# Kernel tuning notes

Measured on AMD Instinct MI355X. Metric: run time of the kernel, lower is better.

## Reference

```python
import jax, jax.numpy as jnp
import numpy as np
from jax import lax

LN_EPS = 1e-6  # flax LayerNorm default


def _layernorm(x, scale, bias):
    mu = jnp.mean(x, axis=-1, keepdims=True)
    var = jnp.mean(jnp.square(x - mu), axis=-1, keepdims=True)
    return (x - mu) * lax.rsqrt(var + LN_EPS) * scale + bias


def _lstm_layer(c0, h0, Wi, Wh, b, x):
    # x: [B, T, F]; carry c/h: [B, H]; gate order i, f, g, o (flax)
    def step(carry, xt):
        c, h = carry
        z = xt @ Wi + h @ Wh + b  # [B, 4H]
        i, f, g, o = jnp.split(z, 4, axis=-1)
        i = jax.nn.sigmoid(i); f = jax.nn.sigmoid(f)
        g = jnp.tanh(g); o = jax.nn.sigmoid(o)
        c = f * c + i * g
        h = o * jnp.tanh(c)
        return (c, h), h
    (cT, hT), hs = lax.scan(step, (c0, h0), jnp.swapaxes(x, 0, 1))
    return cT, hT, jnp.swapaxes(hs, 0, 1)  # hs: [B, T, H]


def setup_inputs() -> dict:
    key = jax.random.key(0)
    ks = jax.random.split(key, 16)
    B, T, F, H, P, A = 64, 128, 512, 1024, 1024, 32
    s = 0.05
    return {
        "x": jax.random.normal(ks[0], (B, T, F), jnp.float32),
        "c0": jnp.zeros((2, B, H), jnp.float32),
        "h0": jnp.zeros((2, B, H), jnp.float32),
        "W_pre": jax.random.normal(ks[1], (F, P), jnp.float32) * s,
        "b_pre": jnp.zeros((P,), jnp.float32),
        "ln_scale": jnp.ones((P,), jnp.float32),
        "ln_bias": jnp.zeros((P,), jnp.float32),
        "Wi0": jax.random.normal(ks[2], (P, 4 * H), jnp.float32) * s,
        "Wh0": jax.random.normal(ks[3], (H, 4 * H), jnp.float32) * s,
        "b0": jnp.zeros((4 * H,), jnp.float32),
        "Wi1": jax.random.normal(ks[4], (H, 4 * H), jnp.float32) * s,
        "Wh1": jax.random.normal(ks[5], (H, 4 * H), jnp.float32) * s,
        "b1": jnp.zeros((4 * H,), jnp.float32),
        "W_post": jax.random.normal(ks[6], (H, P), jnp.float32) * s,
        "b_post": jnp.zeros((P,), jnp.float32),
        "W_out": jax.random.normal(ks[7], (P, A), jnp.float32) * s,
        "b_out": jnp.zeros((A,), jnp.float32),
        "training": False,
    }


def reference(x, c0, h0, W_pre, b_pre, ln_scale, ln_bias,
              Wi0, Wh0, b0, Wi1, Wh1, b1,
              W_post, b_post, W_out, b_out, training):
    # preprocessing: Dense -> LayerNorm -> relu
    h = jax.nn.relu(_layernorm(x @ W_pre + b_pre, ln_scale, ln_bias))
    # two stacked LSTM layers scanned over time
    c1, h1, h = _lstm_layer(c0[0], h0[0], Wi0, Wh0, b0, h)
    c2, h2, h = _lstm_layer(c0[1], h0[1], Wi1, Wh1, b1, h)
    # postprocessing: Dense -> relu (dropout deterministic => identity)
    h = jax.nn.relu(h @ W_post + b_post)
    logits = h @ W_out + b_out  # [B, T, action_dim]
    new_carry = (jnp.stack([c1, c2]), jnp.stack([h1, h2]))
    return new_carry, logits
```

## Files before the change

kernel.cpp:

```cpp
#include <hip/hip_runtime.h>
#include <hip/hip_bf16.h>
#include <math.h>

typedef __attribute__((ext_vector_type(8))) short short8;
typedef __attribute__((ext_vector_type(4))) float f32x4;
typedef __attribute__((ext_vector_type(4))) unsigned u32x4;
typedef unsigned short u16;
typedef unsigned long long u64;

__device__ __forceinline__ u16 f2bf(float f) {
    union { float f; unsigned u; } v; v.f = f;
    unsigned r = v.u + 0x7fffu + ((v.u >> 16) & 1u);
    return (u16)(r >> 16);
}
__device__ __forceinline__ float bf2f(u16 b) {
    union { unsigned u; float f; } v; v.u = ((unsigned)b) << 16;
    return v.f;
}
__device__ __forceinline__ float fast_sigmoid(float x) {
    return __builtin_amdgcn_rcpf(1.f + __expf(-x));
}
__device__ __forceinline__ float fast_tanh(float x) {
    return 1.f - 2.f * __builtin_amdgcn_rcpf(1.f + __expf(2.f * x));
}
__device__ __forceinline__ u32x4 ldg16(const void* p) {
    u32x4 r;
    asm volatile("global_load_dwordx4 %0, %1, off"
                 : "=v"(r) : "v"(p) : "memory");
    return r;
}


__global__ __launch_bounds__(256) void k_zero(unsigned* p, int n) {
    int i = blockIdx.x * 256 + threadIdx.x;
    if (i < n) p[i] = 0u;
}

__global__ __launch_bounds__(256) void k_cvt(const float* __restrict__ in,
                                             u16* __restrict__ out, int n) {
    int i = blockIdx.x * 256 + threadIdx.x;
    if (i < n) out[i] = f2bf(in[i]);
}

__global__ __launch_bounds__(256) void k_cvt_h(const float* __restrict__ in,
                                               u16* __restrict__ out) {
    int i = blockIdx.x * 256 + threadIdx.x;
    int b = i >> 10, j = i & 1023;
    out[(size_t)(j >> 3) * 512 + b * 8 + (j & 7)] = f2bf(in[i]);
}

__global__ __launch_bounds__(256) void k_transpose(const float* __restrict__ W,
                                                   u16* __restrict__ WT, int K, int N) {
    __shared__ float tile[32][33];
    int n0 = blockIdx.x * 32, k0 = blockIdx.y * 32;
    int tx = threadIdx.x & 31, ty = threadIdx.x >> 5;
    #pragma unroll
    for (int j = 0; j < 32; j += 8)
        tile[ty + j][tx] = W[(size_t)(k0 + ty + j) * N + n0 + tx];
    __syncthreads();
    #pragma unroll
    for (int j = 0; j < 32; j += 8)
        WT[(size_t)(n0 + ty + j) * K + k0 + tx] = f2bf(tile[tx][ty + j]);
}

template <int MODE>
__global__ __launch_bounds__(256) void k_gemm(const u16* __restrict__ A,
                                              const u16* __restrict__ BT,
                                              const float* __restrict__ bias,
                                              void* __restrict__ Cout,
                                              int M, int N, int K) {
    const int w = threadIdx.x >> 6, l = threadIdx.x & 63;
    const int lm = l & 15, lq = l >> 4;
    const int r0 = blockIdx.y * 64 + w * 16;
    const int c0 = blockIdx.x * 64;
    const u16* arow = A + (size_t)(r0 + lm) * K + lq * 8;
    const u16* bp0 = BT + (size_t)(c0 + lm) * K + lq * 8;
    const u16* bp1 = bp0 + (size_t)16 * K;
    const u16* bp2 = bp0 + (size_t)32 * K;
    const u16* bp3 = bp0 + (size_t)48 * K;
    f32x4 acc0 = {0.f, 0.f, 0.f, 0.f}, acc1 = acc0, acc2 = acc0, acc3 = acc0;
    for (int k0 = 0; k0 < K; k0 += 32) {
        short8 a = *(const short8*)(arow + k0);
        acc0 = __builtin_amdgcn_mfma_f32_16x16x32_bf16(a, *(const short8*)(bp0 + k0), acc0, 0, 0, 0);
        acc1 = __builtin_amdgcn_mfma_f32_16x16x32_bf16(a, *(const short8*)(bp1 + k0), acc1, 0, 0, 0);
        acc2 = __builtin_amdgcn_mfma_f32_16x16x32_bf16(a, *(const short8*)(bp2 + k0), acc2, 0, 0, 0);
        acc3 = __builtin_amdgcn_mfma_f32_16x16x32_bf16(a, *(const short8*)(bp3 + k0), acc3, 0, 0, 0);
    }
    f32x4 accs[4] = {acc0, acc1, acc2, acc3};
    #pragma unroll
    for (int nt = 0; nt < 4; nt++) {
        #pragma unroll
        for (int r = 0; r < 4; r++) {
            int row = r0 + lq * 4 + r;
            int col = c0 + nt * 16 + lm;
            float v = accs[nt][r] + bias[col];
            if (MODE == 0) {
                ((float*)Cout)[(size_t)row * N + col] = v;
            } else {
                if (MODE == 2) v = fmaxf(v, 0.f);
                ((u16*)Cout)[(size_t)row * N + col] = f2bf(v);
            }
        }
    }
}

__global__ __launch_bounds__(256) void k_ln_relu(const float* __restrict__ X,
                                                 const float* __restrict__ scale,
                                                 const float* __restrict__ bias,
                                                 u16* __restrict__ preS) {
    const int N = 1024;
    int row = blockIdx.x;
    int b = row >> 7, t = row & 127;
    const float* x = X + (size_t)row * N;
    __shared__ float vbuf[1024];
    float s = 0.f, ss = 0.f;
    float vals[4];
    #pragma unroll
    for (int j = 0; j < 4; j++) {
        float v = x[threadIdx.x + 256 * j];
        vals[j] = v; s += v; ss += v * v;
    }
    #pragma unroll
    for (int o = 32; o > 0; o >>= 1) { s += __shfl_down(s, o); ss += __shfl_down(ss, o); }
    __shared__ float rs[4], rss[4];
    int w = threadIdx.x >> 6;
    if ((threadIdx.x & 63) == 0) { rs[w] = s; rss[w] = ss; }
    __syncthreads();
    __shared__ float smu, sinv;
    if (threadIdx.x == 0) {
        float a = rs[0] + rs[1] + rs[2] + rs[3];
        float bq = rss[0] + rss[1] + rss[2] + rss[3];
        float mu = a * (1.f / N);
        float var = bq * (1.f / N) - mu * mu;
        smu = mu; sinv = rsqrtf(var + 1e-6f);
    }
    __syncthreads();
    float mu = smu, inv = sinv;
    #pragma unroll
    for (int j = 0; j < 4; j++) {
        int i = threadIdx.x + 256 * j;
        float v = (vals[j] - mu) * inv * scale[i] + bias[i];
        vbuf[i] = fmaxf(v, 0.f);
    }
    __syncthreads();
    if (threadIdx.x < 128) {
        int g = threadIdx.x;
        union { u16 h[8]; u32x4 v; } pk;
        #pragma unroll
        for (int e = 0; e < 8; e++) pk.h[e] = f2bf(vbuf[g * 8 + e]);
        *(u32x4*)(preS + (size_t)t * 65536 + (size_t)g * 512 + b * 8) = pk.v;
    }
}

#define FBLOCKS 256
__global__ __launch_bounds__(512, 1) void k_lstm_fused(
    const u16* __restrict__ WiT0, const u16* __restrict__ WhT0,
    const u16* __restrict__ WiT1, const u16* __restrict__ WhT1,
    const u16* __restrict__ preS, const float* __restrict__ b0v,
    const float* __restrict__ b1v, const float* __restrict__ c0_all,
    u16* __restrict__ hs0, u16* __restrict__ hs1, u16* __restrict__ Hp,
    float* __restrict__ out, unsigned* __restrict__ ctr) {
    const int bk = blockIdx.x;
    const int role = bk >> 7;
    const int bkl = bk & 127;
    const int tid = threadIdx.x;
    const int w = tid >> 6, l = tid & 63, lm = l & 15, lq = l >> 4;
    const int kp = w >> 2, rt = w & 3;

    __shared__ u16 whs[65536];
    __shared__ float zbuf[2 * 64 * 33];

    {
        const u16* Wx = role ? WiT1 : WiT0;
        const u16* Wh = role ? WhT1 : WhT0;
        for (int f = tid; f < 8192; f += 512) {
            int flm = f & 15, flq = (f >> 4) & 3;
            int fi = (f >> 6) & 31;
            int rest = f >> 11;
            int fg = rest & 1, fkp = (rest >> 1) & 1;
            int lc = fg * 16 + flm;
            int gcolw = (lc >> 3) * 1024 + bkl * 8 + (lc & 7);
            int k = fi * 32 + flq * 8;
            const u16* src = (fkp == 0 ? Wx : Wh) + (size_t)gcolw * 1024 + k;
            *(short8*)(whs + (size_t)f * 8) = *(const short8*)src;
        }
    }
    const int u = tid & 7, b = tid >> 3;
    const int gcol = bkl * 8 + u;
    float c = (c0_all + (size_t)role * 65536)[(size_t)b * 1024 + gcol];
    const float* bv = role ? b1v : b0v;
    float bi0 = bv[gcol], bi1 = bv[1024 + gcol];
    float bi2 = bv[2048 + gcol], bi3 = bv[3072 + gcol];
    u16* hs_my = role ? hs1 : hs0;
    float* c_out = out + (size_t)role * 65536;
    float* h_out = out + 131072 + (size_t)role * 65536;
    const int lanoff = (lq * 16 + lm) * 8;
    __syncthreads();

    for (int t = 0; t < 128; t++) {
        if (tid < 64) {
            if (!role) {
                if (t > 0) {
                    unsigned need = (unsigned)t;
                    for (;;) {
                        unsigned a0 = __hip_atomic_load(&ctr[tid * 16], __ATOMIC_RELAXED,
                                                        __HIP_MEMORY_SCOPE_AGENT);
                        unsigned a1 = __hip_atomic_load(&ctr[(tid + 64) * 16], __ATOMIC_RELAXED,
                                                        __HIP_MEMORY_SCOPE_AGENT);
                        int ok = (a0 >= need) && (a1 >= need);
                        if (__all(ok)) break;
                        __builtin_amdgcn_s_sleep(1);
                    }
                }
            } else {
                unsigned n0 = (unsigned)(t + 1), n1 = (unsigned)t;
                for (;;) {
                    unsigned a0 = __hip_atomic_load(&ctr[tid * 16], __ATOMIC_RELAXED,
                                                    __HIP_MEMORY_SCOPE_AGENT);
                    unsigned a1 = __hip_atomic_load(&ctr[(tid + 64) * 16], __ATOMIC_RELAXED,
                                                    __HIP_MEMORY_SCOPE_AGENT);
                    unsigned b0 = __hip_atomic_load(&ctr[(tid + 128) * 16], __ATOMIC_RELAXED,
                                                    __HIP_MEMORY_SCOPE_AGENT);
                    unsigned b1 = __hip_atomic_load(&ctr[(tid + 192) * 16], __ATOMIC_RELAXED,
                                                    __HIP_MEMORY_SCOPE_AGENT);
                    int ok = (a0 >= n0) && (a1 >= n0) && (b0 >= n1) && (b1 >= n1);
                    if (__all(ok)) break;
                    __builtin_amdgcn_s_sleep(1);
                }
            }
        }
        __syncthreads();

        const u16* abase;
        if (!role) abase = (kp == 0) ? preS + (size_t)t * 65536
                                     : hs0 + (size_t)t * 65536;
        else       abase = (kp == 0) ? hs0 + (size_t)(t + 1) * 65536
                                     : hs1 + (size_t)t * 65536;
        const u16* arow = abase + (size_t)lq * 512 + (rt * 16 + lm) * 8;
        const u16* bw0 = whs + kp * 32768 + lanoff;

        f32x4 acc0 = {0.f, 0.f, 0.f, 0.f}, acc1 = acc0;
        #define STEPF(Ai, i)                                                      \
        {   union { u32x4 q; short8 v; } _a; _a.q = (Ai);                         \
            short8 _b0 = *(const short8*)(bw0 + (i) * 512);                       \
            short8 _b1 = *(const short8*)(bw0 + 16384 + (i) * 512);               \
            acc0 = __builtin_amdgcn_mfma_f32_16x16x32_bf16(_a.v, _b0, acc0, 0, 0, 0); \
            acc1 = __builtin_amdgcn_mfma_f32_16x16x32_bf16(_a.v, _b1, acc1, 0, 0, 0); }

        u32x4 A0 = ldg16(arow +     0), A1 = ldg16(arow +  2048);
        u32x4 A2 = ldg16(arow +  4096), A3 = ldg16(arow +  6144);
        u32x4 A4 = ldg16(arow +  8192), A5 = ldg16(arow + 10240);
        u32x4 A6 = ldg16(arow + 12288), A7 = ldg16(arow + 14336);
        u32x4 A8 = ldg16(arow + 16384), A9 = ldg16(arow + 18432);
        u32x4 A10 = ldg16(arow + 20480), A11 = ldg16(arow + 22528);
        u32x4 A12 = ldg16(arow + 24576), A13 = ldg16(arow + 26624);
        u32x4 A14 = ldg16(arow + 28672), A15 = ldg16(arow + 30720);
        u32x4 A16 = ldg16(arow + 32768), A17 = ldg16(arow + 34816);
        u32x4 A18 = ldg16(arow + 36864), A19 = ldg16(arow + 38912);
        u32x4 A20 = ldg16(arow + 40960), A21 = ldg16(arow + 43008);
        u32x4 A22 = ldg16(arow + 45056), A23 = ldg16(arow + 47104);
        u32x4 A24 = ldg16(arow + 49152), A25 = ldg16(arow + 51200);
        u32x4 A26 = ldg16(arow + 53248), A27 = ldg16(arow + 55296);
        u32x4 A28 = ldg16(arow + 57344), A29 = ldg16(arow + 59392);
        u32x4 A30 = ldg16(arow + 61440), A31 = ldg16(arow + 63488);
        asm volatile("s_waitcnt vmcnt(24)"
                     : "+v"(A0), "+v"(A1), "+v"(A2), "+v"(A3),
                       "+v"(A4), "+v"(A5), "+v"(A6), "+v"(A7) :: "memory");
        STEPF(A0, 0) STEPF(A1, 1) STEPF(A2, 2) STEPF(A3, 3)
        STEPF(A4, 4) STEPF(A5, 5) STEPF(A6, 6) STEPF(A7, 7)
        asm volatile("s_waitcnt vmcnt(16)"
                     : "+v"(A8), "+v"(A9), "+v"(A10), "+v"(A11),
                       "+v"(A12), "+v"(A13), "+v"(A14), "+v"(A15) :: "memory");
        STEPF(A8, 8) STEPF(A9, 9) STEPF(A10, 10) STEPF(A11, 11)
        STEPF(A12, 12) STEPF(A13, 13) STEPF(A14, 14) STEPF(A15, 15)
        asm volatile("s_waitcnt vmcnt(8)"
                     : "+v"(A16), "+v"(A17), "+v"(A18), "+v"(A19),
                       "+v"(A20), "+v"(A21), "+v"(A22), "+v"(A23) :: "memory");
        STEPF(A16, 16) STEPF(A17, 17) STEPF(A18, 18) STEPF(A19, 19)
        STEPF(A20, 20) STEPF(A21, 21) STEPF(A22, 22) STEPF(A23, 23)
        asm volatile("s_waitcnt vmcnt(0)"
                     : "+v"(A24), "+v"(A25), "+v"(A26), "+v"(A27),
                       "+v"(A28), "+v"(A29), "+v"(A30), "+v"(A31) :: "memory");
        STEPF(A24, 24) STEPF(A25, 25) STEPF(A26, 26) STEPF(A27, 27)
        STEPF(A28, 28) STEPF(A29, 29) STEPF(A30, 30) STEPF(A31, 31)
        #undef STEPF

        {
            float* zb = zbuf + (size_t)kp * 2112;
            #pragma unroll
            for (int r = 0; r < 4; r++) {
                int row = rt * 16 + lq * 4 + r;
                zb[row * 33 + lm] = acc0[r];
                zb[row * 33 + 16 + lm] = acc1[r];
            }
        }
        __syncthreads();

        {
            const float* z0 = zbuf + (size_t)b * 33;
            const float* z1 = z0 + 2112;
            float gi = z0[u]      + z1[u]      + bi0;
            float gf = z0[8 + u]  + z1[8 + u]  + bi1;
            float gg = z0[16 + u] + z1[16 + u] + bi2;
            float go = z0[24 + u] + z1[24 + u] + bi3;
            gi = fast_sigmoid(gi);
            gf = fast_sigmoid(gf);
            gg = fast_tanh(gg);
            go = fast_sigmoid(go);
            c = gf * c + gi * gg;
            float h = go * fast_tanh(c);
            unsigned hv = (unsigned)f2bf(h);
            int base = l & 56;
            unsigned p0 = __shfl(hv, base + 0, 64) | (__shfl(hv, base + 1, 64) << 16);
            unsigned p1 = __shfl(hv, base + 2, 64) | (__shfl(hv, base + 3, 64) << 16);
            unsigned p2 = __shfl(hv, base + 4, 64) | (__shfl(hv, base + 5, 64) << 16);
            unsigned p3 = __shfl(hv, base + 6, 64) | (__shfl(hv, base + 7, 64) << 16);
            if (u == 0) {
                u32x4 pv = {p0, p1, p2, p3};
                u16* dst = hs_my + (size_t)(t + 1) * 65536 + (size_t)bkl * 512 + b * 8;
                asm volatile("global_store_dwordx4 %0, %1, off sc0 sc1"
                             :: "v"(dst), "v"(pv) : "memory");
                if (role) {
                    u16* d2 = Hp + (size_t)(t * 64 + b) * 1024 + bkl * 8;
                    *(u32x4*)d2 = pv;
                }
            }
            if (t == 127) {
                c_out[(size_t)b * 1024 + gcol] = c;
                h_out[(size_t)b * 1024 + gcol] = h;
            }
        }
        __syncthreads();

        if (tid == 0)
            __hip_atomic_store(&ctr[bk * 16], (unsigned)(t + 1), __ATOMIC_RELAXED,
                               __HIP_MEMORY_SCOPE_AGENT);
    }
}

__global__ __launch_bounds__(256) void k_logits(const u16* __restrict__ Pact,
                                                const u16* __restrict__ WoT,
                                                const float* __restrict__ bout,
                                                float* __restrict__ out) {
    int r = blockIdx.x * 8 + (threadIdx.x >> 5);
    int n = threadIdx.x & 31;
    const u16* a = Pact + (size_t)r * 1024;
    const u16* wv = WoT + (size_t)n * 1024;
    float s = 0.f;
    for (int k = 0; k < 1024; k += 8) {
        short8 av = *(const short8*)(a + k);
        short8 wvv = *(const short8*)(wv + k);
        #pragma unroll
        for (int j = 0; j < 8; j++)
            s += bf2f((u16)av[j]) * bf2f((u16)wvv[j]);
    }
    int t = r >> 6, b = r & 63;
    out[((size_t)b * 128 + t) * 32 + n] = s + bout[n];
}

extern "C" void kernel_launch(void* const* d_in, const int* in_sizes, int n_in,
                              void* d_out, int out_size, void* d_ws, size_t ws_size,
                              hipStream_t stream) {
    const float* x      = (const float*)d_in[0];
    const float* c0     = (const float*)d_in[1];
    const float* h0     = (const float*)d_in[2];
    const float* W_pre  = (const float*)d_in[3];
    const float* b_pre  = (const float*)d_in[4];
    const float* ln_s   = (const float*)d_in[5];
    const float* ln_b   = (const float*)d_in[6];
    const float* Wi0    = (const float*)d_in[7];
    const float* Wh0    = (const float*)d_in[8];
    const float* b0     = (const float*)d_in[9];
    const float* Wi1    = (const float*)d_in[10];
    const float* Wh1    = (const float*)d_in[11];
    const float* b1     = (const float*)d_in[12];
    const float* W_post = (const float*)d_in[13];
    const float* b_post = (const float*)d_in[14];
    const float* W_out  = (const float*)d_in[15];
    const float* b_out  = (const float*)d_in[16];
    float* out = (float*)d_out;

    char* ws = (char*)d_ws;
    size_t off = 0;
    auto alloc = [&](size_t bytes) {
        void* p = ws + off;
        off += (bytes + 255) & ~(size_t)255;
        return p;
    };
    u16* WTpre  = (u16*)alloc((size_t)1024 * 512 * 2);
    u16* WTi0   = (u16*)alloc((size_t)4096 * 1024 * 2);
    u16* WTh0   = (u16*)alloc((size_t)4096 * 1024 * 2);
    u16* WTi1   = (u16*)alloc((size_t)4096 * 1024 * 2);
    u16* WTh1   = (u16*)alloc((size_t)4096 * 1024 * 2);
    u16* WTpost = (u16*)alloc((size_t)1024 * 1024 * 2);
    u16* WTout  = (u16*)alloc((size_t)32 * 1024 * 2);
    u16* Xb     = (u16*)alloc((size_t)8192 * 512 * 2);
    u16* preS   = (u16*)alloc((size_t)128 * 65536 * 2);
    u16* hs0    = (u16*)alloc((size_t)129 * 65536 * 2);
    u16* hs1    = (u16*)alloc((size_t)129 * 65536 * 2);
    u16* postact= (u16*)alloc((size_t)8192 * 1024 * 2);
    unsigned* ctr = (unsigned*)alloc(32768);
    void* unionreg = alloc((size_t)8192 * 4096 * 2);
    float* pre_f32 = (float*)unionreg;
    u16* Hplain = (u16*)unionreg;

    k_zero<<<32, 256, 0, stream>>>(ctr, 8192);
    k_cvt<<<(8192 * 512) / 256, 256, 0, stream>>>(x, Xb, 8192 * 512);
    k_cvt_h<<<256, 256, 0, stream>>>(h0, hs0);
    k_cvt_h<<<256, 256, 0, stream>>>(h0 + 65536, hs1);

    k_transpose<<<dim3(32, 16), 256, 0, stream>>>(W_pre, WTpre, 512, 1024);
    k_transpose<<<dim3(128, 32), 256, 0, stream>>>(Wi0, WTi0, 1024, 4096);
    k_transpose<<<dim3(128, 32), 256, 0, stream>>>(Wh0, WTh0, 1024, 4096);
    k_transpose<<<dim3(128, 32), 256, 0, stream>>>(Wi1, WTi1, 1024, 4096);
    k_transpose<<<dim3(128, 32), 256, 0, stream>>>(Wh1, WTh1, 1024, 4096);
    k_transpose<<<dim3(32, 32), 256, 0, stream>>>(W_post, WTpost, 1024, 1024);
    k_transpose<<<dim3(1, 32), 256, 0, stream>>>(W_out, WTout, 1024, 32);

    k_gemm<0><<<dim3(16, 128), 256, 0, stream>>>(Xb, WTpre, b_pre, pre_f32, 8192, 1024, 512);
    k_ln_relu<<<8192, 256, 0, stream>>>(pre_f32, ln_s, ln_b, preS);

    {
        const u16* WiT0_ = WTi0; const u16* WhT0_ = WTh0;
        const u16* WiT1_ = WTi1; const u16* WhT1_ = WTh1;
        const u16* preS_ = preS; const float* b0_ = b0; const float* b1_ = b1;
        const float* c0_ = c0; u16* hs0_ = hs0; u16* hs1_ = hs1;
        u16* Hp_ = Hplain; float* out_ = out; unsigned* ctr_ = ctr;
        void* args[] = {&WiT0_, &WhT0_, &WiT1_, &WhT1_, &preS_, &b0_, &b1_,
                        &c0_, &hs0_, &hs1_, &Hp_, &out_, &ctr_};
        hipLaunchCooperativeKernel((void*)k_lstm_fused, dim3(FBLOCKS), dim3(512),
                                   args, 0, stream);
    }

    k_gemm<2><<<dim3(16, 128), 256, 0, stream>>>(Hplain, WTpost, b_post, postact,
                                                 8192, 1024, 1024);
    k_logits<<<1024, 256, 0, stream>>>(postact, WTout, b_out, out + 262144);
}
```

Measured before the change: 1.171 ms.

## Aggregate step counters into striped fetch-add slots and drop pre-GEMM block barrier

Replaces the per-block step flags, which every waiting block polled across 128 or 256 counters, with 16 striped counters that each block fetch-adds. Each wave now polls only the 8 counters it depends on, and only when its own K-half actually needs that data. The __syncthreads after the wait is removed, so each wave proceeds independently, and the MFMA section runs at raised wave priority. This is meant to cut spin-poll traffic and barrier latency on the serial recurrence path, at the cost of atomic contention on the shared counters. The code that zeroes the counters must match the new scheme.

```diff
diff --git a/kernel.cpp b/kernel.cpp
--- a/kernel.cpp
+++ b/kernel.cpp
@@ -198,38 +198,25 @@
     __syncthreads();
 
     for (int t = 0; t < 128; t++) {
-        if (tid < 64) {
+        {
+            unsigned need = 0; int base = 0; int dowait = 0;
             if (!role) {
-                if (t > 0) {
-                    unsigned need = (unsigned)t;
-                    for (;;) {
-                        unsigned a0 = __hip_atomic_load(&ctr[tid * 16], __ATOMIC_RELAXED,
-                                                        __HIP_MEMORY_SCOPE_AGENT);
-                        unsigned a1 = __hip_atomic_load(&ctr[(tid + 64) * 16], __ATOMIC_RELAXED,
-                                                        __HIP_MEMORY_SCOPE_AGENT);
-                        int ok = (a0 >= need) && (a1 >= need);
-                        if (__all(ok)) break;
-                        __builtin_amdgcn_s_sleep(1);
-                    }
-                }
+                if (kp == 1 && t > 0) { need = 16u * (unsigned)t; base = 0; dowait = 1; }
             } else {
-                unsigned n0 = (unsigned)(t + 1), n1 = (unsigned)t;
+                if (kp == 0)          { need = 16u * (unsigned)(t + 1); base = 0; dowait = 1; }
+                else if (t > 0)       { need = 16u * (unsigned)t; base = 8; dowait = 1; }
+            }
+            if (dowait) {
                 for (;;) {
-                    unsigned a0 = __hip_atomic_load(&ctr[tid * 16], __ATOMIC_RELAXED,
-                                                    __HIP_MEMORY_SCOPE_AGENT);
-                    unsigned a1 = __hip_atomic_load(&ctr[(tid + 64) * 16], __ATOMIC_RELAXED,
-                                                    __HIP_MEMORY_SCOPE_AGENT);
-                    unsigned b0 = __hip_atomic_load(&ctr[(tid + 128) * 16], __ATOMIC_RELAXED,
-                                                    __HIP_MEMORY_SCOPE_AGENT);
-                    unsigned b1 = __hip_atomic_load(&ctr[(tid + 192) * 16], __ATOMIC_RELAXED,
-                                                    __HIP_MEMORY_SCOPE_AGENT);
-                    int ok = (a0 >= n0) && (a1 >= n0) && (b0 >= n1) && (b1 >= n1);
-                    if (__all(ok)) break;
+                    unsigned v = need;
+                    if (l < 8)
+                        v = __hip_atomic_load(&ctr[(base + l) * 16], __ATOMIC_RELAXED,
+                                              __HIP_MEMORY_SCOPE_AGENT);
+                    if (__all((int)(v >= need))) break;
                     __builtin_amdgcn_s_sleep(1);
                 }
             }
         }
-        __syncthreads();
 
         const u16* abase;
         if (!role) abase = (kp == 0) ? preS + (size_t)t * 65536
@@ -263,6 +250,7 @@
         u32x4 A26 = ldg16(arow + 53248), A27 = ldg16(arow + 55296);
         u32x4 A28 = ldg16(arow + 57344), A29 = ldg16(arow + 59392);
         u32x4 A30 = ldg16(arow + 61440), A31 = ldg16(arow + 63488);
+        __builtin_amdgcn_s_setprio(1);
         asm volatile("s_waitcnt vmcnt(24)"
                      : "+v"(A0), "+v"(A1), "+v"(A2), "+v"(A3),
                        "+v"(A4), "+v"(A5), "+v"(A6), "+v"(A7) :: "memory");
@@ -283,6 +271,7 @@
                        "+v"(A28), "+v"(A29), "+v"(A30), "+v"(A31) :: "memory");
         STEPF(A24, 24) STEPF(A25, 25) STEPF(A26, 26) STEPF(A27, 27)
         STEPF(A28, 28) STEPF(A29, 29) STEPF(A30, 30) STEPF(A31, 31)
+        __builtin_amdgcn_s_setprio(0);
         #undef STEPF
 
         {
@@ -333,8 +322,8 @@
         __syncthreads();
 
         if (tid == 0)
-            __hip_atomic_store(&ctr[bk * 16], (unsigned)(t + 1), __ATOMIC_RELAXED,
-                               __HIP_MEMORY_SCOPE_AGENT);
+            __hip_atomic_fetch_add(&ctr[(role * 8 + (bkl & 7)) * 16], 1u,
+                                   __ATOMIC_RELAXED, __HIP_MEMORY_SCOPE_AGENT);
     }
 }
 
```

Result: no change. 1.186 ms (+1.2%).
